# Optimization experiments

Hardware: AMD Instinct MI355X
Metric: run time of the kernel (lower is better)

The kernel has to match this reference:

```python
import jax, jax.numpy as jnp
import numpy as np

B = 64            # number of graphs in the batch
D = 128           # in_node_dim
NUM_VIEWS = 4
MAX_NODES = 508   # max(node_counts) for the deterministic counts below


def _make_counts():
    # deterministic ragged node counts: 256, 260, ..., 508
    return jnp.asarray(256 + 4 * np.arange(B), dtype=jnp.int64)


def setup_inputs() -> dict:
    key = jax.random.key(0)
    node_counts = _make_counts()
    total = int(np.sum(256 + 4 * np.arange(B)))  # 24448
    z_nodes = jax.random.normal(key, (total, D), dtype=jnp.float32)
    return {"z_nodes": z_nodes, "node_counts": node_counts}


def reference(z_nodes, node_counts):
    # Pad ragged node embeddings into a dense [B, MAX_NODES, D] block with
    # zero rows for padding; then padded z @ z^T directly equals the
    # zero-padded per-graph adjacency logits (outer products with zero rows
    # are zero), matching the torch loop + torch.zeros pad.
    offsets = jnp.concatenate([jnp.zeros((1,), node_counts.dtype),
                               jnp.cumsum(node_counts)[:-1]])          # [B]
    pos = jnp.arange(MAX_NODES)                                        # [M]
    valid = pos[None, :] < node_counts[:, None]                        # [B, M]
    idx = jnp.where(valid, offsets[:, None] + pos[None, :], 0)         # [B, M]
    z_pad = z_nodes[idx] * valid[..., None].astype(z_nodes.dtype)      # [B, M, D]
    adj = jnp.einsum('bnd,bmd->bnm', z_pad, z_pad)                     # [B, M, M]
    # unsqueeze(1).repeat(1, V, 1, 1)
    return jnp.broadcast_to(adj[:, None], (B, NUM_VIEWS, MAX_NODES, MAX_NODES))
```

## Files before the change

### kernel.cpp

```cpp
#include <hip/hip_runtime.h>
#include <stdint.h>


typedef __bf16          v8bf __attribute__((ext_vector_type(8)));
typedef unsigned short  v8us __attribute__((ext_vector_type(8)));
typedef float           v4f  __attribute__((ext_vector_type(4)));
typedef unsigned int    v4u  __attribute__((ext_vector_type(4)));

#define NMAX 508
#define DD   128
#define NV   4
#define LDC  132

__device__ __forceinline__ unsigned short f32_to_bf16_rne(float f) {
    unsigned int u = __builtin_bit_cast(unsigned int, f);
    u = (u + 0x7fffu + ((u >> 16) & 1u)) >> 16;
    return (unsigned short)u;
}

__device__ __forceinline__ v8bf cvt8(v4f lo, v4f hi) {
    v8us u;
    u[0] = f32_to_bf16_rne(lo.x); u[1] = f32_to_bf16_rne(lo.y);
    u[2] = f32_to_bf16_rne(lo.z); u[3] = f32_to_bf16_rne(lo.w);
    u[4] = f32_to_bf16_rne(hi.x); u[5] = f32_to_bf16_rne(hi.y);
    u[6] = f32_to_bf16_rne(hi.z); u[7] = f32_to_bf16_rne(hi.w);
    return __builtin_bit_cast(v8bf, u);
}

__global__ __launch_bounds__(256, 4)
void adj_gram_kernel(const float* __restrict__ z,
                     const int*   __restrict__ counts,
                     float*       __restrict__ out)
{
    __shared__ __align__(16) float sC[64 * LDC];

    const int blk = blockIdx.x;
    const int b   = blk >> 5;
    const int ti  = (blk >> 2) & 7;
    const int tj  = blk & 3;
    const int i0  = ti * 64;
    const int j0  = tj * 128;

    const int tid  = threadIdx.x;
    const int lane = tid & 63;
    const int wave = tid >> 6;

    const bool is64 = (counts[1] == 0);
    int cnt = is64 ? counts[2 * lane] : counts[lane];
    int inc = cnt;
    #pragma unroll
    for (int s = 1; s < 64; s <<= 1) {
        int t = __shfl_up(inc, s);
        if (lane >= s) inc += t;
    }
    const int n   = __shfl(cnt, b);
    const int off = __shfl(inc, b) - n;

    const int nx = wave * 32;
    const int lr = lane & 15;
    const int lk = (lane >> 4) * 8;

    v4f acc[4][2];
    #pragma unroll
    for (int mt = 0; mt < 4; ++mt)
        #pragma unroll
        for (int nt = 0; nt < 2; ++nt) acc[mt][nt] = (v4f)0.0f;

    if (i0 < n && j0 < n) {
        const float* zb = z + (size_t)off * DD;
        #pragma unroll
        for (int ks = 0; ks < 4; ++ks) {
            const int ko = ks * 32 + lk;
            v8bf af[4], bfv[2];
            #pragma unroll
            for (int mt = 0; mt < 4; ++mt) {
                const int r = i0 + mt * 16 + lr;
                v4f lo = (v4f)0.0f, hi = (v4f)0.0f;
                if (r < n) {
                    const float* p = zb + (size_t)r * DD + ko;
                    lo = *(const v4f*)p;
                    hi = *(const v4f*)(p + 4);
                }
                af[mt] = cvt8(lo, hi);
            }
            #pragma unroll
            for (int nt = 0; nt < 2; ++nt) {
                const int r = j0 + nx + nt * 16 + lr;
                v4f lo = (v4f)0.0f, hi = (v4f)0.0f;
                if (r < n) {
                    const float* p = zb + (size_t)r * DD + ko;
                    lo = *(const v4f*)p;
                    hi = *(const v4f*)(p + 4);
                }
                bfv[nt] = cvt8(lo, hi);
            }
            #pragma unroll
            for (int mt = 0; mt < 4; ++mt)
                #pragma unroll
                for (int nt = 0; nt < 2; ++nt)
                    acc[mt][nt] = __builtin_amdgcn_mfma_f32_16x16x32_bf16(
                        af[mt], bfv[nt], acc[mt][nt], 0, 0, 0);
        }
    }

    const int crow = (lane >> 4) * 4;
    #pragma unroll
    for (int mt = 0; mt < 4; ++mt)
        #pragma unroll
        for (int nt = 0; nt < 2; ++nt)
            #pragma unroll
            for (int rr = 0; rr < 4; ++rr)
                sC[(mt * 16 + crow + rr) * LDC + nx + nt * 16 + lr] = acc[mt][nt][rr];
    __syncthreads();

    const int rs = tid >> 5;
    const int cs = tid & 31;
    const int gc = j0 + cs * 4;
    #pragma unroll
    for (int it = 0; it < 8; ++it) {
        const int r  = it * 8 + rs;
        const int gr = i0 + r;
        if (gr >= NMAX || gc >= NMAX) continue;
        const v4u v = *(const v4u*)&sC[r * LDC + cs * 4];
        const size_t rowbase = (size_t)gr * NMAX + gc;
        #pragma unroll
        for (int vv = 0; vv < NV; ++vv) {
            const size_t o = (size_t)(b * NV + vv) * (size_t)(NMAX * NMAX) + rowbase;
            *(v4u*)(out + o) = v;
        }
    }
}

extern "C" void kernel_launch(void* const* d_in, const int* in_sizes, int n_in,
                              void* d_out, int out_size, void* d_ws, size_t ws_size,
                              hipStream_t stream) {
    const float* z      = (const float*)d_in[0];
    const int*   counts = (const int*)d_in[1];
    float*       out    = (float*)d_out;
    adj_gram_kernel<<<dim3(64 * 32), dim3(256), 0, stream>>>(z, counts, out);
}
```

Measured before the change: 327.2 us.

## Retile to full-width 16-row stripes with contiguous, 128B-aligned output stores

Each block now computes a 16-row by full-width stripe of the Gram matrix, with each wave covering 128 columns, instead of a 64x128 tile. The stripe is written out as one contiguous run per view. The store loop is aligned to 8-vector (128-byte) boundaries so the write-bound output phase produces full, coalesced lines rather than partial 508-column row fragments. In exchange the A-operand is reused less, each wave loads more B rows, and the store loop adds an integer divide per vector.

```diff
diff --git a/kernel.cpp b/kernel.cpp
--- a/kernel.cpp
+++ b/kernel.cpp
@@ -7,10 +7,13 @@
 typedef float           v4f  __attribute__((ext_vector_type(4)));
 typedef unsigned int    v4u  __attribute__((ext_vector_type(4)));
 
-#define NMAX 508
-#define DD   128
-#define NV   4
-#define LDC  132
+#define NMAX  508
+#define DD    128
+#define NV    4
+#define IMG   (NMAX * NMAX)
+#define IMGV4 (IMG / 4)
+#define ROWV4 (NMAX / 4)
+#define LDS2  516
 
 __device__ __forceinline__ unsigned short f32_to_bf16_rne(float f) {
     unsigned int u = __builtin_bit_cast(unsigned int, f);
@@ -32,18 +35,17 @@
                      const int*   __restrict__ counts,
                      float*       __restrict__ out)
 {
-    __shared__ __align__(16) float sC[64 * LDC];
+    __shared__ __align__(16) float sC[16 * LDS2];
 
     const int blk = blockIdx.x;
     const int b   = blk >> 5;
-    const int ti  = (blk >> 2) & 7;
-    const int tj  = blk & 3;
-    const int i0  = ti * 64;
-    const int j0  = tj * 128;
+    const int sl  = blk & 31;
+    const int i0  = sl * 16;
 
     const int tid  = threadIdx.x;
     const int lane = tid & 63;
     const int wave = tid >> 6;
+    const int j0   = wave * 128;
 
     const bool is64 = (counts[1] == 0);
     int cnt = is64 ? counts[2 * lane] : counts[lane];
@@ -56,36 +58,32 @@
     const int n   = __shfl(cnt, b);
     const int off = __shfl(inc, b) - n;
 
-    const int nx = wave * 32;
     const int lr = lane & 15;
     const int lk = (lane >> 4) * 8;
 
-    v4f acc[4][2];
+    v4f acc[8];
     #pragma unroll
-    for (int mt = 0; mt < 4; ++mt)
-        #pragma unroll
-        for (int nt = 0; nt < 2; ++nt) acc[mt][nt] = (v4f)0.0f;
+    for (int nt = 0; nt < 8; ++nt) acc[nt] = (v4f)0.0f;
 
-    if (i0 < n && j0 < n) {
+    if (i0 < n) {
         const float* zb = z + (size_t)off * DD;
         #pragma unroll
         for (int ks = 0; ks < 4; ++ks) {
             const int ko = ks * 32 + lk;
-            v8bf af[4], bfv[2];
-            #pragma unroll
-            for (int mt = 0; mt < 4; ++mt) {
-                const int r = i0 + mt * 16 + lr;
+            v8bf af, bfv[8];
+            {
+                const int r = i0 + lr;
                 v4f lo = (v4f)0.0f, hi = (v4f)0.0f;
                 if (r < n) {
                     const float* p = zb + (size_t)r * DD + ko;
                     lo = *(const v4f*)p;
                     hi = *(const v4f*)(p + 4);
                 }
-                af[mt] = cvt8(lo, hi);
+                af = cvt8(lo, hi);
             }
             #pragma unroll
-            for (int nt = 0; nt < 2; ++nt) {
-                const int r = j0 + nx + nt * 16 + lr;
+            for (int nt = 0; nt < 8; ++nt) {
+                const int r = j0 + nt * 16 + lr;
                 v4f lo = (v4f)0.0f, hi = (v4f)0.0f;
                 if (r < n) {
                     const float* p = zb + (size_t)r * DD + ko;
@@ -95,38 +93,33 @@
                 bfv[nt] = cvt8(lo, hi);
             }
             #pragma unroll
-            for (int mt = 0; mt < 4; ++mt)
-                #pragma unroll
-                for (int nt = 0; nt < 2; ++nt)
-                    acc[mt][nt] = __builtin_amdgcn_mfma_f32_16x16x32_bf16(
-                        af[mt], bfv[nt], acc[mt][nt], 0, 0, 0);
+            for (int nt = 0; nt < 8; ++nt)
+                acc[nt] = __builtin_amdgcn_mfma_f32_16x16x32_bf16(
+                    af, bfv[nt], acc[nt], 0, 0, 0);
         }
     }
 
     const int crow = (lane >> 4) * 4;
     #pragma unroll
-    for (int mt = 0; mt < 4; ++mt)
+    for (int nt = 0; nt < 8; ++nt)
         #pragma unroll
-        for (int nt = 0; nt < 2; ++nt)
-            #pragma unroll
-            for (int rr = 0; rr < 4; ++rr)
-                sC[(mt * 16 + crow + rr) * LDC + nx + nt * 16 + lr] = acc[mt][nt][rr];
+        for (int rr = 0; rr < 4; ++rr)
+            sC[(crow + rr) * LDS2 + j0 + nt * 16 + lr] = acc[nt][rr];
     __syncthreads();
 
-    const int rs = tid >> 5;
-    const int cs = tid & 31;
-    const int gc = j0 + cs * 4;
-    #pragma unroll
-    for (int it = 0; it < 8; ++it) {
-        const int r  = it * 8 + rs;
-        const int gr = i0 + r;
-        if (gr >= NMAX || gc >= NMAX) continue;
-        const v4u v = *(const v4u*)&sC[r * LDC + cs * 4];
-        const size_t rowbase = (size_t)gr * NMAX + gc;
-        #pragma unroll
-        for (int vv = 0; vv < NV; ++vv) {
-            const size_t o = (size_t)(b * NV + vv) * (size_t)(NMAX * NMAX) + rowbase;
-            *(v4u*)(out + o) = v;
+    const int rowsv = (NMAX - i0 < 16) ? (NMAX - i0) : 16;
+    const int nvec  = rowsv * ROWV4;
+    for (int v = 0; v < NV; ++v) {
+        const size_t G0 = (size_t)(b * NV + v) * IMGV4 + (size_t)i0 * ROWV4;
+        const size_t Ga = G0 & ~(size_t)7;
+        const size_t G1 = G0 + (size_t)nvec;
+        for (size_t g = Ga + tid; g < G1; g += 256) {
+            if (g < G0) continue;
+            const int f   = (int)(g - G0);
+            const int row = f / ROWV4;
+            const int c4  = f - row * ROWV4;
+            const v4u val = *(const v4u*)&sC[row * LDS2 + c4 * 4];
+            *(v4u*)(out + g * 4) = val;
         }
     }
 }
```

New measurement: 295.3 us. -9.7%, faster.
